# Performance work log

Hardware: AMD Instinct MI355X
Metric: run time of the kernel (lower is better)

Reference implementation:

```python
import math
import jax, jax.numpy as jnp
import numpy as np

H = 1024
NH = 16
HD = H // NH
FF = 4096


def gelu_erf(x):
    return x * 0.5 * (1.0 + jax.lax.erf(x / jnp.sqrt(jnp.float32(2.0))))


def layernorm(x, gamma, beta, eps=1e-12):
    mean = x.mean(axis=-1, keepdims=True)
    var = ((x - mean) ** 2).mean(axis=-1, keepdims=True)
    return gamma * (x - mean) / jnp.sqrt(var + eps) + beta


def setup_inputs() -> dict:
    key = jax.random.key(0)
    ks = jax.random.split(key, 12)
    B, S = 2, 2048
    sc = 0.02
    return {
        "x": jax.random.normal(ks[0], (B, S, H), jnp.float32),
        "attention_mask": jnp.ones((B, S), jnp.int32),
        "Wq": jax.random.normal(ks[1], (H, H), jnp.float32) * sc,
        "bq": jnp.zeros((H,), jnp.float32),
        "Wk": jax.random.normal(ks[2], (H, H), jnp.float32) * sc,
        "bk": jnp.zeros((H,), jnp.float32),
        "Wv": jax.random.normal(ks[3], (H, H), jnp.float32) * sc,
        "bv": jnp.zeros((H,), jnp.float32),
        "Wo": jax.random.normal(ks[4], (H, H), jnp.float32) * sc,
        "bo": jnp.zeros((H,), jnp.float32),
        "ln1_g": jnp.ones((H,), jnp.float32),
        "ln1_b": jnp.zeros((H,), jnp.float32),
        "W1": jax.random.normal(ks[5], (H, FF), jnp.float32) * sc,
        "b1": jnp.zeros((FF,), jnp.float32),
        "W2": jax.random.normal(ks[6], (FF, H), jnp.float32) * sc,
        "b2": jnp.zeros((H,), jnp.float32),
        "ln2_g": jnp.ones((H,), jnp.float32),
        "ln2_b": jnp.zeros((H,), jnp.float32),
    }


def reference(x, attention_mask, Wq, bq, Wk, bk, Wv, bv, Wo, bo,
              ln1_g, ln1_b, W1, b1, W2, b2, ln2_g, ln2_b):
    B, S, _ = x.shape
    # QKV projections, split heads -> [B, NH, S, HD]
    def split(t):
        return t.reshape(B, S, NH, HD).transpose(0, 2, 1, 3)
    q = split(x @ Wq + bq)
    k = split(x @ Wk + bk)
    v = split(x @ Wv + bv)
    # scores [B, NH, S, S]
    s = jnp.einsum("bhqd,bhkd->bhqk", q, k) / math.sqrt(HD)
    mask = (attention_mask == 1)[:, None, None, :]  # [B,1,1,S]
    s = jnp.where(mask, s, -jnp.inf)
    p = jax.nn.softmax(s, axis=-1)
    a = jnp.einsum("bhqk,bhkd->bhqd", p, v)
    a = a.transpose(0, 2, 1, 3).reshape(B, S, H)  # merge heads
    a = a @ Wo + bo
    a = layernorm(a, ln1_g, ln1_b)  # NOTE: no residual in source
    m = gelu_erf(a @ W1 + b1) @ W2 + b2
    return layernorm(m, ln2_g, ln2_b)
```

## Files before the change

kernel.cpp:

```cpp
#include <hip/hip_runtime.h>
#include <hip/hip_bf16.h>
#include <math.h>

typedef __bf16 bf16;
typedef __attribute__((ext_vector_type(8))) __bf16 bf16x8;
typedef __attribute__((ext_vector_type(4))) __bf16 bf16x4;
typedef __attribute__((ext_vector_type(2))) __bf16 bf16x2;
typedef __attribute__((ext_vector_type(4))) float f32x4;
typedef __attribute__((ext_vector_type(4))) short short4v;

#define HDIM 1024
#define NHEAD 16
#define HD 64
#define FFDIM 4096
#define BATCH 2
#define SEQ 2048
#define M_TOK 4096
#define NSPLIT 4
#define PSTRIDE ((size_t)M_TOK * HDIM)

static __device__ __forceinline__ void async_load16(const bf16* g, bf16* l) {
  __builtin_amdgcn_global_load_lds(
      (const __attribute__((address_space(1))) void*)g,
      (__attribute__((address_space(3))) void*)l, 16, 0, 0);
}

static __device__ __forceinline__ f32x4 mfma16_bf16(bf16x4 a, bf16x4 b, f32x4 c) {
#if defined(__HIP_DEVICE_COMPILE__)
#if __has_builtin(__builtin_amdgcn_mfma_f32_16x16x16bf16_1k)
  return __builtin_amdgcn_mfma_f32_16x16x16bf16_1k(
      __builtin_bit_cast(short4v, a), __builtin_bit_cast(short4v, b), c, 0, 0, 0);
#else
  return __builtin_amdgcn_mfma_f32_16x16x16_bf16(a, b, c, 0, 0, 0);
#endif
#else
  return c;
#endif
}

__global__ __launch_bounds__(256)
void prep_kernel(const float* __restrict__ x,
                 const float* __restrict__ Wq, const float* __restrict__ Wk,
                 const float* __restrict__ Wv, const float* __restrict__ Wo,
                 const float* __restrict__ W1, const float* __restrict__ W2,
                 bf16* __restrict__ Xb, bf16* __restrict__ QKVT,
                 bf16* __restrict__ W1T, bf16* __restrict__ W2T)
{
  const int z = blockIdx.z;
  const int t = threadIdx.x;
  if (z == 12) {
    const size_t base = ((size_t)(blockIdx.y * 32 + blockIdx.x)) * 4096;
#pragma unroll
    for (int j = 0; j < 4; ++j) {
      const size_t i = base + j * 1024 + t * 4;
      f32x4 v = *(const f32x4*)(x + i);
      bf16x4 o;
#pragma unroll
      for (int k = 0; k < 4; ++k) o[k] = (bf16)v[k];
      *(bf16x4*)(Xb + i) = o;
    }
    return;
  }
  const float* ps; bf16* pd; int sld, dld;
  if (z < 4) {
    ps = (z == 0) ? Wq : (z == 1) ? Wk : (z == 2) ? Wv : Wo;
    pd = QKVT + (size_t)z * HDIM * HDIM; sld = 1024; dld = 1024;
  } else if (z < 8) {
    const int c = z - 4;
    ps = W1 + c * 1024; sld = 4096;
    pd = W1T + (size_t)c * 1024 * 1024; dld = 1024;
  } else {
    const int c = z - 8;
    ps = W2 + (size_t)c * 1024 * 1024; sld = 1024;
    pd = W2T + c * 1024; dld = 4096;
  }
  __shared__ float tile[32][33];
  const int tx = t & 31, ty = t >> 5;
  const int c0 = blockIdx.x * 32, r0 = blockIdx.y * 32;
#pragma unroll
  for (int i = 0; i < 32; i += 8)
    tile[ty + i][tx] = ps[(size_t)(r0 + ty + i) * sld + c0 + tx];
  __syncthreads();
  const int rr0 = (t & 15) * 2;
  const int ccb = t >> 4;
#pragma unroll
  for (int i = 0; i < 2; ++i) {
    const int cc = ccb + 16 * i;
    bf16x2 v = {(bf16)tile[rr0][cc], (bf16)tile[rr0 + 1][cc]};
    *(bf16x2*)(pd + (size_t)(c0 + cc) * dld + r0 + rr0) = v;
  }
}

template<int EPI>
__global__ __launch_bounds__(256)
void gemm_bt(const bf16* __restrict__ A, const bf16* __restrict__ Bt,
             const float* __restrict__ b0, const float* __restrict__ b1p,
             const float* __restrict__ b2p, void* __restrict__ Cout,
             int M, int N, int ldk, int kchunk)
{
  __shared__ __align__(16) bf16 As[128 * 64];
  __shared__ __align__(16) bf16 Bs[128 * 64];
  const int t = threadIdx.x;
  const int wave = t >> 6, lane = t & 63;
  const int lm = lane & 15, qd = lane >> 4;
  const int wm = (wave >> 1) * 64, wn = (wave & 1) * 64;
  const int bm = blockIdx.y * 128, bn = blockIdx.x * 128;
  const int kbeg = blockIdx.z * kchunk;

  f32x4 acc[4][4] = {};
  const int srow = t >> 3;
  const int schk = t & 7;

  for (int k0 = kbeg; k0 < kbeg + kchunk; k0 += 64) {
#pragma unroll
    for (int r = 0; r < 4; ++r) {
      const int row = r * 32 + srow;
      const int chunk = schk ^ (row & 7);
      async_load16(A + (size_t)(bm + row) * ldk + (k0 + chunk * 8),
                   (bf16*)((char*)As + r * 4096 + t * 16));
    }
#pragma unroll
    for (int r = 0; r < 4; ++r) {
      const int row = r * 32 + srow;
      const int chunk = schk ^ (row & 7);
      async_load16(Bt + (size_t)(bn + row) * ldk + (k0 + chunk * 8),
                   (bf16*)((char*)Bs + r * 4096 + t * 16));
    }
    __syncthreads();
#pragma unroll
    for (int ks = 0; ks < 2; ++ks) {
      bf16x8 av[4], bv[4];
#pragma unroll
      for (int mt = 0; mt < 4; ++mt) {
        const int row = wm + mt * 16 + lm;
        const int chunk = (ks * 4 + qd) ^ (row & 7);
        av[mt] = *(const bf16x8*)(As + row * 64 + chunk * 8);
      }
#pragma unroll
      for (int nt = 0; nt < 4; ++nt) {
        const int row = wn + nt * 16 + lm;
        const int chunk = (ks * 4 + qd) ^ (row & 7);
        bv[nt] = *(const bf16x8*)(Bs + row * 64 + chunk * 8);
      }
#pragma unroll
      for (int mt = 0; mt < 4; ++mt)
#pragma unroll
        for (int nt = 0; nt < 4; ++nt)
          acc[mt][nt] = __builtin_amdgcn_mfma_f32_16x16x32_bf16(bv[nt], av[mt], acc[mt][nt], 0, 0, 0);
    }
    __syncthreads();
  }

#pragma unroll
  for (int nt = 0; nt < 4; ++nt) {
    const int n0 = bn + wn + nt * 16 + qd * 4;
    f32x4 bsv = {0.f, 0.f, 0.f, 0.f};
    if (EPI == 2) bsv = *(const f32x4*)(b0 + n0);
    if (EPI == 3) {
      const int sect = n0 >> 10, c = n0 & 1023;
      const float* bp = (sect == 0) ? b0 : (sect == 1) ? b1p : b2p;
      bsv = *(const f32x4*)(bp + c);
    }
#pragma unroll
    for (int mt = 0; mt < 4; ++mt) {
      const int m = bm + wm + mt * 16 + lm;
      f32x4 v;
#pragma unroll
      for (int r = 0; r < 4; ++r) v[r] = acc[mt][nt][r] + bsv[r];
      if (EPI == 1) {
        bf16x4 o;
#pragma unroll
        for (int r = 0; r < 4; ++r) o[r] = (bf16)v[r];
        *(bf16x4*)((bf16*)Cout + (size_t)blockIdx.z * M * N + (size_t)m * N + n0) = o;
      } else if (EPI == 2) {
        bf16x4 o;
#pragma unroll
        for (int r = 0; r < 4; ++r) {
          const float z = v[r] * 0.70710678118f;
          const float az = fabsf(z);
          const float tt = __builtin_amdgcn_rcpf(fmaf(az, 0.3275911f, 1.0f));
          const float poly = tt * fmaf(tt, fmaf(tt, fmaf(tt, fmaf(tt, 1.061405429f,
                             -1.453152027f), 1.421413741f), -0.284496736f), 0.254829592f);
          const float e = __builtin_amdgcn_exp2f(az * az * -1.4426950408889634f);
          float erfv = 1.0f - poly * e;
          erfv = (z < 0.f) ? -erfv : erfv;
          o[r] = (bf16)(0.5f * v[r] * (1.0f + erfv));
        }
        *(bf16x4*)((bf16*)Cout + (size_t)m * N + n0) = o;
      } else {
        bf16* base = (bf16*)Cout;
        const int sect = n0 >> 10, c = n0 & 1023;
        if (sect < 2) {
          bf16x4 o;
#pragma unroll
          for (int r = 0; r < 4; ++r) o[r] = (bf16)v[r];
          *(bf16x4*)(base + (size_t)sect * M_TOK * HDIM + (size_t)m * HDIM + c) = o;
        } else {
          const int hh = c >> 6, dd = c & 63;
          const int bb = m >> 11, ss = m & 2047;
#pragma unroll
          for (int r = 0; r < 4; ++r)
            base[(size_t)2 * M_TOK * HDIM +
                 (size_t)((bb * NHEAD + hh) * HD + dd + r) * SEQ + ss] = (bf16)v[r];
        }
      }
    }
  }
}

__global__ __launch_bounds__(256)
void attn_kernel(const bf16* __restrict__ Q, const bf16* __restrict__ Kg,
                 const bf16* __restrict__ Vt, const int* __restrict__ mask,
                 bf16* __restrict__ Po, float* __restrict__ Lp)
{
  __shared__ __align__(16) bf16 Ks[64 * 64];
  __shared__ __align__(16) bf16 Vs[64 * 64];
  __shared__ float madd[64];

  const int t = threadIdx.x;
  const int wave = t >> 6, lane = t & 63;
  const int lm = lane & 15, qd = lane >> 4;

  const int lin = blockIdx.x;
  const int g = (lin & 7) * 16 + (lin >> 7);
  const int qblk = (lin >> 3) & 15;
  const int bh = g >> 2;
  const int split = g & 3;
  const int b = bh >> 4, h = bh & 15;
  const int q0 = qblk * 128 + wave * 32;
  const int kv_beg = split * (SEQ / NSPLIT);

  bf16x8 qf[2][2];
#pragma unroll
  for (int qt = 0; qt < 2; ++qt)
#pragma unroll
    for (int ks = 0; ks < 2; ++ks)
      qf[qt][ks] = *(const bf16x8*)(Q + (size_t)(b * SEQ + q0 + qt * 16 + lm) * HDIM +
                                    h * HD + ks * 32 + qd * 8);

  const bf16 onev = (bf16)1.0f;
  const bf16x4 ones = {onev, onev, onev, onev};
  f32x4 lacc[2] = {};
  f32x4 oacc[2][4] = {};

  const int srow = t >> 3, schk = t & 7;
  const float C = 0.1803368801f;

  for (int kv0 = kv_beg; kv0 < kv_beg + SEQ / NSPLIT; kv0 += 64) {
#pragma unroll
    for (int r = 0; r < 2; ++r) {
      const int row = r * 32 + srow;
      const int g2 = schk ^ (row & 7);
      async_load16(Kg + (size_t)(b * SEQ + kv0 + row) * HDIM + h * HD + g2 * 8,
                   (bf16*)((char*)Ks + r * 4096 + t * 16));
      async_load16(Vt + (size_t)(bh * HD + row) * SEQ + kv0 + g2 * 8,
                   (bf16*)((char*)Vs + r * 4096 + t * 16));
    }
    if (t < 64) madd[t] = (mask[b * SEQ + kv0 + t] == 1) ? 0.f : -1.0e30f;
    __syncthreads();

    bf16x8 kf[2][4];
#pragma unroll
    for (int ks = 0; ks < 2; ++ks)
#pragma unroll
      for (int nt = 0; nt < 4; ++nt) {
        const int row = nt * 16 + lm;
        const int c = (ks * 4 + qd) ^ (row & 7);
        kf[ks][nt] = *(const bf16x8*)(Ks + row * 64 + c * 8);
      }

    bf16x4 pf[2][4];
#pragma unroll
    for (int qt = 0; qt < 2; ++qt) {
      f32x4 sacc[4] = {};
#pragma unroll
      for (int ks = 0; ks < 2; ++ks)
#pragma unroll
        for (int nt = 0; nt < 4; ++nt)
          sacc[nt] = __builtin_amdgcn_mfma_f32_16x16x32_bf16(kf[ks][nt], qf[qt][ks], sacc[nt], 0, 0, 0);
#pragma unroll
      for (int nt = 0; nt < 4; ++nt) {
        f32x4 ma = *(const f32x4*)(madd + nt * 16 + qd * 4);
#pragma unroll
        for (int r = 0; r < 4; ++r)
          pf[qt][nt][r] = (bf16)__builtin_amdgcn_exp2f(fmaf(sacc[nt][r], C, ma[r]));
        lacc[qt] = mfma16_bf16(ones, pf[qt][nt], lacc[qt]);
      }
    }

#pragma unroll
    for (int nt2 = 0; nt2 < 4; ++nt2) {
      const int row = nt2 * 16 + lm;
#pragma unroll
      for (int nt = 0; nt < 4; ++nt) {
        bf16x4 vf = *(const bf16x4*)(Vs + row * 64 +
                     (((nt * 2 + (qd >> 1)) ^ (row & 7)) * 8) + (qd & 1) * 4);
        oacc[0][nt2] = mfma16_bf16(vf, pf[0][nt], oacc[0][nt2]);
        oacc[1][nt2] = mfma16_bf16(vf, pf[1][nt], oacc[1][nt2]);
      }
    }
    __syncthreads();
  }

  bf16* po = Po + (size_t)(split * 32 + bh) * 64 * SEQ;
#pragma unroll
  for (int qt = 0; qt < 2; ++qt) {
#pragma unroll
    for (int nt2 = 0; nt2 < 4; ++nt2)
#pragma unroll
      for (int r = 0; r < 4; ++r)
        po[(size_t)(nt2 * 16 + qd * 4 + r) * SEQ + q0 + qt * 16 + lm] =
            (bf16)oacc[qt][nt2][r];
    if (qd == 0)
      Lp[(size_t)(split * 32 + bh) * SEQ + q0 + qt * 16 + lm] = lacc[qt][0];
  }
}

__global__ __launch_bounds__(256)
void attn_merge(const bf16* __restrict__ Po, const float* __restrict__ Lp,
                bf16* __restrict__ Aout)
{
  __shared__ bf16 tile[64][80];
  __shared__ float linv[64];
  const int t = threadIdx.x;
  const int bh = blockIdx.y;
  const int b = bh >> 4, h = bh & 15;
  const int s0 = blockIdx.x * 64;

  if (t < 64) {
    float l = 0.f;
#pragma unroll
    for (int s = 0; s < NSPLIT; ++s)
      l += Lp[(size_t)(s * 32 + bh) * SEQ + s0 + t];
    linv[t] = 1.0f / l;
  }
  __syncthreads();

#pragma unroll
  for (int it = 0; it < 2; ++it) {
    const int d = (t >> 3) + 32 * it;
    const int sc = (t & 7) * 8;
    float acc[8] = {};
#pragma unroll
    for (int s = 0; s < NSPLIT; ++s) {
      bf16x8 v = *(const bf16x8*)(Po + ((size_t)(s * 32 + bh) * 64 + d) * SEQ + s0 + sc);
#pragma unroll
      for (int j = 0; j < 8; ++j) acc[j] += (float)v[j];
    }
#pragma unroll
    for (int j = 0; j < 8; ++j)
      tile[sc + j][d] = (bf16)(acc[j] * linv[sc + j]);
  }
  __syncthreads();

  const int tok = t >> 2, dc = (t & 3) * 16;
  bf16x8 o0 = *(const bf16x8*)&tile[tok][dc];
  bf16x8 o1 = *(const bf16x8*)&tile[tok][dc + 8];
  bf16* dst = Aout + (size_t)(b * SEQ + s0 + tok) * HDIM + h * HD + dc;
  *(bf16x8*)dst = o0;
  *(bf16x8*)(dst + 8) = o1;
}

template<int NP, int OUT_BF16>
__global__ __launch_bounds__(256)
void ln_sum(const bf16* __restrict__ p, const float* __restrict__ bias,
            const float* __restrict__ gamma, const float* __restrict__ beta,
            void* __restrict__ out)
{
  const int row = blockIdx.x;
  const int t = threadIdx.x;
  f32x4 v = {0.f, 0.f, 0.f, 0.f};
#pragma unroll
  for (int np = 0; np < NP; ++np) {
    bf16x4 u = *(const bf16x4*)(p + np * PSTRIDE + (size_t)row * HDIM + t * 4);
#pragma unroll
    for (int j = 0; j < 4; ++j) v[j] += (float)u[j];
  }
  f32x4 bv0 = *(const f32x4*)(bias + t * 4);
#pragma unroll
  for (int j = 0; j < 4; ++j) v[j] += bv0[j];

  float s = v[0] + v[1] + v[2] + v[3];
  float s2 = v[0] * v[0] + v[1] * v[1] + v[2] * v[2] + v[3] * v[3];
#pragma unroll
  for (int d = 1; d < 64; d <<= 1) { s += __shfl_xor(s, d, 64); s2 += __shfl_xor(s2, d, 64); }
  __shared__ float ss[4], ss2[4];
  const int wave = t >> 6, lane = t & 63;
  if (lane == 0) { ss[wave] = s; ss2[wave] = s2; }
  __syncthreads();
  s = ss[0] + ss[1] + ss[2] + ss[3];
  s2 = ss2[0] + ss2[1] + ss2[2] + ss2[3];
  const float mean = s * (1.0f / HDIM);
  const float var = s2 * (1.0f / HDIM) - mean * mean;
  const float rstd = rsqrtf(var + 1e-12f);
  f32x4 gv = *(const f32x4*)(gamma + t * 4);
  f32x4 bv = *(const f32x4*)(beta + t * 4);
  f32x4 y;
#pragma unroll
  for (int j = 0; j < 4; ++j) y[j] = gv[j] * (v[j] - mean) * rstd + bv[j];
  if (OUT_BF16) {
    bf16x4 o;
#pragma unroll
    for (int j = 0; j < 4; ++j) o[j] = (bf16)y[j];
    *(bf16x4*)((bf16*)out + (size_t)row * HDIM + t * 4) = o;
  } else {
    *(f32x4*)((float*)out + (size_t)row * HDIM + t * 4) = y;
  }
}

extern "C" void kernel_launch(void* const* d_in, const int* in_sizes, int n_in,
                              void* d_out, int out_size, void* d_ws, size_t ws_size,
                              hipStream_t stream)
{
  const float* x    = (const float*)d_in[0];
  const int*   am   = (const int*)d_in[1];
  const float* Wq   = (const float*)d_in[2];
  const float* bq   = (const float*)d_in[3];
  const float* Wk   = (const float*)d_in[4];
  const float* bk   = (const float*)d_in[5];
  const float* Wv   = (const float*)d_in[6];
  const float* bv   = (const float*)d_in[7];
  const float* Wo   = (const float*)d_in[8];
  const float* bo   = (const float*)d_in[9];
  const float* ln1g = (const float*)d_in[10];
  const float* ln1b = (const float*)d_in[11];
  const float* W1   = (const float*)d_in[12];
  const float* b1   = (const float*)d_in[13];
  const float* W2   = (const float*)d_in[14];
  const float* b2   = (const float*)d_in[15];
  const float* ln2g = (const float*)d_in[16];
  const float* ln2b = (const float*)d_in[17];

  char* ws = (char*)d_ws;
  const size_t MB = 1ull << 20;
  bf16*  W1T  = (bf16*)(ws + 0 * MB);
  bf16*  W2T  = (bf16*)(ws + 8 * MB);
  bf16*  Xb   = (bf16*)(ws + 16 * MB);
  bf16*  QKVT = (bf16*)(ws + 24 * MB);
  bf16*  WoT  = QKVT + (size_t)3 * HDIM * HDIM;
  bf16*  Qb   = (bf16*)(ws + 33 * MB);
  bf16*  Kb   = (bf16*)(ws + 41 * MB);
  bf16*  Vtb  = (bf16*)(ws + 49 * MB);
  bf16*  Po   = (bf16*)(ws + 57 * MB);
  float* Lp   = (float*)(ws + 89 * MB);
  bf16*  Ab   = (bf16*)(ws + 16 * MB);
  bf16*  Pw   = (bf16*)(ws + 33 * MB);
  bf16*  L1   = (bf16*)(ws + 65 * MB);
  bf16*  F1   = (bf16*)(ws + 16 * MB);
  bf16*  Pf   = (bf16*)(ws + 48 * MB);

  prep_kernel<<<dim3(32, 32, 13), 256, 0, stream>>>(x, Wq, Wk, Wv, Wo, W1, W2,
                                                    Xb, QKVT, W1T, W2T);

  gemm_bt<3><<<dim3(3072 / 128, M_TOK / 128, 1), 256, 0, stream>>>(
      Xb, QKVT, bq, bk, bv, Qb, M_TOK, 3072, HDIM, HDIM);

  attn_kernel<<<dim3(2048, 1, 1), 256, 0, stream>>>(Qb, Kb, Vtb, am, Po, Lp);
  attn_merge<<<dim3(SEQ / 64, BATCH * NHEAD), 256, 0, stream>>>(Po, Lp, Ab);

  gemm_bt<1><<<dim3(HDIM / 128, M_TOK / 128, 2), 256, 0, stream>>>(
      Ab, WoT, nullptr, nullptr, nullptr, Pw, M_TOK, HDIM, HDIM, 512);
  ln_sum<2, 1><<<M_TOK, 256, 0, stream>>>(Pw, bo, ln1g, ln1b, L1);

  gemm_bt<2><<<dim3(FFDIM / 128, M_TOK / 128, 1), 256, 0, stream>>>(
      L1, W1T, b1, nullptr, nullptr, F1, M_TOK, FFDIM, HDIM, HDIM);

  gemm_bt<1><<<dim3(HDIM / 128, M_TOK / 128, 4), 256, 0, stream>>>(
      F1, W2T, nullptr, nullptr, nullptr, Pf, M_TOK, HDIM, FFDIM, 1024);
  ln_sum<4, 0><<<M_TOK, 256, 0, stream>>>(Pf, b2, ln2g, ln2b, (float*)d_out);
}
```

Baseline: 362.2 us.

## Replace 128x128 GEMM with double-buffered 256x256 pipelined MFMA kernel

Replaces the single-buffered 128x128 GEMM with a 512-thread kernel that computes 256x256 output tiles. It double-buffers LDS and interleaves async global-to-LDS staging of the next K-tile with four MFMA phases, using explicit barriers, vmcnt waits and s_setprio. The larger tiles raise operand reuse and the overlap hides load latency behind math. In exchange, grids shrink to 128–256 blocks, which may underfill the 256 CUs (especially the Wo projection). The 128KB of LDS per block also limits residency to one block per CU.

```diff
diff --git a/kernel.cpp b/kernel.cpp
--- a/kernel.cpp
+++ b/kernel.cpp
@@ -91,69 +91,126 @@
   }
 }
 
+
+#define STAGE_Q(OP, BASEMN, LDSB, KOFF, Q) do { \
+    const int rr_ = (Q) * 64 + (t >> 3); \
+    const int gc_ = (t & 7) ^ (rr_ & 7); \
+    async_load16((OP) + (size_t)((BASEMN) + rr_) * ldk + (KOFF) + gc_ * 8, \
+                 (LDSB) + (Q) * 4096 + t * 8); \
+  } while (0)
+
+#define STAGE_HALF(OP, BASEMN, LDSB, KOFF, H) do { \
+    STAGE_Q(OP, BASEMN, LDSB, KOFF, 2 * (H)); \
+    STAGE_Q(OP, BASEMN, LDSB, KOFF, 2 * (H) + 1); \
+  } while (0)
+
+#define LOAD_AV(BUF, MH) do { \
+    _Pragma("unroll") \
+    for (int mt_ = 0; mt_ < 4; ++mt_) { \
+      const int row_ = wm + (MH) * 64 + mt_ * 16 + lm; \
+      _Pragma("unroll") \
+      for (int ks_ = 0; ks_ < 2; ++ks_) { \
+        const int c_ = (ks_ * 4 + qd) ^ (row_ & 7); \
+        av[mt_][ks_] = *(const bf16x8*)(As_[BUF] + row_ * 64 + c_ * 8); \
+      } \
+    } \
+  } while (0)
+
+#define LOAD_BV(DST, BUF, NH) do { \
+    _Pragma("unroll") \
+    for (int nt_ = 0; nt_ < 2; ++nt_) { \
+      const int row_ = wnb + (NH) * 32 + nt_ * 16 + lm; \
+      _Pragma("unroll") \
+      for (int ks_ = 0; ks_ < 2; ++ks_) { \
+        const int c_ = (ks_ * 4 + qd) ^ (row_ & 7); \
+        DST[nt_][ks_] = *(const bf16x8*)(Bs_[BUF] + row_ * 64 + c_ * 8); \
+      } \
+    } \
+  } while (0)
+
+#define MFMA_Q(MH, BV, NH) do { \
+    __builtin_amdgcn_s_setprio(1); \
+    _Pragma("unroll") \
+    for (int mt_ = 0; mt_ < 4; ++mt_) \
+      _Pragma("unroll") \
+      for (int nt_ = 0; nt_ < 2; ++nt_) \
+        _Pragma("unroll") \
+        for (int ks_ = 0; ks_ < 2; ++ks_) \
+          acc[(MH) * 4 + mt_][(NH) * 2 + nt_] = \
+              __builtin_amdgcn_mfma_f32_16x16x32_bf16( \
+                  BV[nt_][ks_], av[mt_][ks_], \
+                  acc[(MH) * 4 + mt_][(NH) * 2 + nt_], 0, 0, 0); \
+    __builtin_amdgcn_s_setprio(0); \
+  } while (0)
+
+#define BARX() do { \
+    __builtin_amdgcn_sched_barrier(0); \
+    __builtin_amdgcn_s_barrier(); \
+    __builtin_amdgcn_sched_barrier(0); \
+  } while (0)
+
+#define VMCNT4() asm volatile("s_waitcnt vmcnt(4)" ::: "memory")
+
+#define FOURPH(RB, WAB, KTA, WBB, KTB) do { \
+     \
+    LOAD_AV(RB, 0); LOAD_BV(bv0, RB, 0); \
+    STAGE_HALF(A, bm, As_[WAB], kbeg + (KTA) * 64, 0); \
+    BARX(); MFMA_Q(0, bv0, 0); BARX(); \
+     \
+    LOAD_BV(bv1, RB, 1); \
+    STAGE_HALF(A, bm, As_[WAB], kbeg + (KTA) * 64, 1); \
+    BARX(); MFMA_Q(0, bv1, 1); BARX(); \
+     \
+    LOAD_AV(RB, 1); \
+    STAGE_HALF(Bt, bn, Bs_[WBB], kbeg + (KTB) * 64, 0); \
+    BARX(); MFMA_Q(1, bv0, 0); BARX(); \
+     \
+    STAGE_HALF(Bt, bn, Bs_[WBB], kbeg + (KTB) * 64, 1); \
+    BARX(); MFMA_Q(1, bv1, 1); VMCNT4(); BARX(); \
+  } while (0)
+
 template<int EPI>
-__global__ __launch_bounds__(256)
-void gemm_bt(const bf16* __restrict__ A, const bf16* __restrict__ Bt,
+__global__ __launch_bounds__(512, 2)
+void gemm256(const bf16* __restrict__ A, const bf16* __restrict__ Bt,
              const float* __restrict__ b0, const float* __restrict__ b1p,
              const float* __restrict__ b2p, void* __restrict__ Cout,
              int M, int N, int ldk, int kchunk)
 {
-  __shared__ __align__(16) bf16 As[128 * 64];
-  __shared__ __align__(16) bf16 Bs[128 * 64];
+  __shared__ __align__(16) bf16 As_[2][256 * 64];
+  __shared__ __align__(16) bf16 Bs_[2][256 * 64];
+
   const int t = threadIdx.x;
   const int wave = t >> 6, lane = t & 63;
   const int lm = lane & 15, qd = lane >> 4;
-  const int wm = (wave >> 1) * 64, wn = (wave & 1) * 64;
-  const int bm = blockIdx.y * 128, bn = blockIdx.x * 128;
+  const int wm = (wave >> 2) * 128;
+  const int wnb = (wave & 3) * 64;
+  const int bm = blockIdx.y * 256, bn = blockIdx.x * 256;
   const int kbeg = blockIdx.z * kchunk;
-
-  f32x4 acc[4][4] = {};
-  const int srow = t >> 3;
-  const int schk = t & 7;
-
-  for (int k0 = kbeg; k0 < kbeg + kchunk; k0 += 64) {
-#pragma unroll
-    for (int r = 0; r < 4; ++r) {
-      const int row = r * 32 + srow;
-      const int chunk = schk ^ (row & 7);
-      async_load16(A + (size_t)(bm + row) * ldk + (k0 + chunk * 8),
-                   (bf16*)((char*)As + r * 4096 + t * 16));
-    }
-#pragma unroll
-    for (int r = 0; r < 4; ++r) {
-      const int row = r * 32 + srow;
-      const int chunk = schk ^ (row & 7);
-      async_load16(Bt + (size_t)(bn + row) * ldk + (k0 + chunk * 8),
-                   (bf16*)((char*)Bs + r * 4096 + t * 16));
-    }
-    __syncthreads();
-#pragma unroll
-    for (int ks = 0; ks < 2; ++ks) {
-      bf16x8 av[4], bv[4];
-#pragma unroll
-      for (int mt = 0; mt < 4; ++mt) {
-        const int row = wm + mt * 16 + lm;
-        const int chunk = (ks * 4 + qd) ^ (row & 7);
-        av[mt] = *(const bf16x8*)(As + row * 64 + chunk * 8);
-      }
-#pragma unroll
-      for (int nt = 0; nt < 4; ++nt) {
-        const int row = wn + nt * 16 + lm;
-        const int chunk = (ks * 4 + qd) ^ (row & 7);
-        bv[nt] = *(const bf16x8*)(Bs + row * 64 + chunk * 8);
-      }
-#pragma unroll
-      for (int mt = 0; mt < 4; ++mt)
-#pragma unroll
-        for (int nt = 0; nt < 4; ++nt)
-          acc[mt][nt] = __builtin_amdgcn_mfma_f32_16x16x32_bf16(bv[nt], av[mt], acc[mt][nt], 0, 0, 0);
-    }
-    __syncthreads();
-  }
-
-#pragma unroll
-  for (int nt = 0; nt < 4; ++nt) {
-    const int n0 = bn + wn + nt * 16 + qd * 4;
+  const int NT = kchunk >> 6;
+
+  f32x4 acc[8][4] = {};
+  bf16x8 av[4][2], bv0[2][2], bv1[2][2];
+
+  STAGE_HALF(Bt, bn, Bs_[0], kbeg, 0);
+  STAGE_HALF(Bt, bn, Bs_[0], kbeg, 1);
+  STAGE_HALF(A,  bm, As_[0], kbeg, 0);
+  STAGE_HALF(A,  bm, As_[0], kbeg, 1);
+  STAGE_HALF(Bt, bn, Bs_[1], kbeg + 64, 0);
+  STAGE_HALF(Bt, bn, Bs_[1], kbeg + 64, 1);
+  VMCNT4();
+  BARX();
+
+  for (int it = 0; it < NT / 2; ++it) {
+    const int tb = 2 * it + 1;
+    const int tc = (2 * it + 2) & (NT - 1);
+    const int td = (2 * it + 3) & (NT - 1);
+    FOURPH(0, 1, tb, 0, tc);
+    FOURPH(1, 0, tc, 1, td);
+  }
+
+#pragma unroll
+  for (int nt4 = 0; nt4 < 4; ++nt4) {
+    const int n0 = bn + wnb + nt4 * 16 + qd * 4;
     f32x4 bsv = {0.f, 0.f, 0.f, 0.f};
     if (EPI == 2) bsv = *(const f32x4*)(b0 + n0);
     if (EPI == 3) {
@@ -162,11 +219,11 @@
       bsv = *(const f32x4*)(bp + c);
     }
 #pragma unroll
-    for (int mt = 0; mt < 4; ++mt) {
-      const int m = bm + wm + mt * 16 + lm;
+    for (int mt8 = 0; mt8 < 8; ++mt8) {
+      const int m = bm + wm + mt8 * 16 + lm;
       f32x4 v;
 #pragma unroll
-      for (int r = 0; r < 4; ++r) v[r] = acc[mt][nt][r] + bsv[r];
+      for (int r = 0; r < 4; ++r) v[r] = acc[mt8][nt4][r] + bsv[r];
       if (EPI == 1) {
         bf16x4 o;
 #pragma unroll
@@ -452,20 +509,20 @@
   prep_kernel<<<dim3(32, 32, 13), 256, 0, stream>>>(x, Wq, Wk, Wv, Wo, W1, W2,
                                                     Xb, QKVT, W1T, W2T);
 
-  gemm_bt<3><<<dim3(3072 / 128, M_TOK / 128, 1), 256, 0, stream>>>(
+  gemm256<3><<<dim3(3072 / 256, M_TOK / 256, 1), 512, 0, stream>>>(
       Xb, QKVT, bq, bk, bv, Qb, M_TOK, 3072, HDIM, HDIM);
 
   attn_kernel<<<dim3(2048, 1, 1), 256, 0, stream>>>(Qb, Kb, Vtb, am, Po, Lp);
   attn_merge<<<dim3(SEQ / 64, BATCH * NHEAD), 256, 0, stream>>>(Po, Lp, Ab);
 
-  gemm_bt<1><<<dim3(HDIM / 128, M_TOK / 128, 2), 256, 0, stream>>>(
+  gemm256<1><<<dim3(HDIM / 256, M_TOK / 256, 2), 512, 0, stream>>>(
       Ab, WoT, nullptr, nullptr, nullptr, Pw, M_TOK, HDIM, HDIM, 512);
   ln_sum<2, 1><<<M_TOK, 256, 0, stream>>>(Pw, bo, ln1g, ln1b, L1);
 
-  gemm_bt<2><<<dim3(FFDIM / 128, M_TOK / 128, 1), 256, 0, stream>>>(
+  gemm256<2><<<dim3(FFDIM / 256, M_TOK / 256, 1), 512, 0, stream>>>(
       L1, W1T, b1, nullptr, nullptr, F1, M_TOK, FFDIM, HDIM, HDIM);
 
-  gemm_bt<1><<<dim3(HDIM / 128, M_TOK / 128, 4), 256, 0, stream>>>(
+  gemm256<1><<<dim3(HDIM / 256, M_TOK / 256, 4), 512, 0, stream>>>(
       F1, W2T, nullptr, nullptr, nullptr, Pf, M_TOK, HDIM, FFDIM, 1024);
   ln_sum<4, 0><<<M_TOK, 256, 0, stream>>>(Pf, b2, ln2g, ln2b, (float*)d_out);
 }
```

Measured after the change: 358.2 us. About the same (-1.1%).

## Stage GEMM epilogue through LDS, halve attention KV splits, add MFMA priority hints

Applied to the files above, without the earlier changes.

The GEMM epilogue now writes each wave's 64x64 output tile into shared memory first, then stores it to global memory as full 16-byte rows. This includes the transposed V layout, which previously used scattered 2-byte stores. Attention drops from four KV splits to two, halving the grid and the partial outputs that the merge step must read. s_setprio is raised around the MFMA sections to favour matrix issue. The risks are lower attention parallelism from the smaller grid, and extra LDS traffic plus possible bank conflicts in the epilogue.

```diff
diff --git a/kernel.cpp b/kernel.cpp
--- a/kernel.cpp
+++ b/kernel.cpp
@@ -16,7 +16,7 @@
 #define BATCH 2
 #define SEQ 2048
 #define M_TOK 4096
-#define NSPLIT 4
+#define NSPLIT 2
 #define PSTRIDE ((size_t)M_TOK * HDIM)
 
 static __device__ __forceinline__ void async_load16(const bf16* g, bf16* l) {
@@ -98,8 +98,9 @@
              const float* __restrict__ b2p, void* __restrict__ Cout,
              int M, int N, int ldk, int kchunk)
 {
-  __shared__ __align__(16) bf16 As[128 * 64];
-  __shared__ __align__(16) bf16 Bs[128 * 64];
+  __shared__ __align__(16) bf16 Smem[2][128 * 64];
+  bf16* As = Smem[0];
+  bf16* Bs = Smem[1];
   const int t = threadIdx.x;
   const int wave = t >> 6, lane = t & 63;
   const int lm = lane & 15, qd = lane >> 4;
@@ -150,6 +151,9 @@
     }
     __syncthreads();
   }
+
+  bf16* tw = &Smem[0][0] + wave * 4096;
+  const bool vt = (EPI == 3) && ((bn + wn) >= 2 * HDIM);
 
 #pragma unroll
   for (int nt = 0; nt < 4; ++nt) {
@@ -163,17 +167,11 @@
     }
 #pragma unroll
     for (int mt = 0; mt < 4; ++mt) {
-      const int m = bm + wm + mt * 16 + lm;
       f32x4 v;
 #pragma unroll
       for (int r = 0; r < 4; ++r) v[r] = acc[mt][nt][r] + bsv[r];
-      if (EPI == 1) {
-        bf16x4 o;
-#pragma unroll
-        for (int r = 0; r < 4; ++r) o[r] = (bf16)v[r];
-        *(bf16x4*)((bf16*)Cout + (size_t)blockIdx.z * M * N + (size_t)m * N + n0) = o;
-      } else if (EPI == 2) {
-        bf16x4 o;
+      bf16x4 o;
+      if (EPI == 2) {
 #pragma unroll
         for (int r = 0; r < 4; ++r) {
           const float z = v[r] * 0.70710678118f;
@@ -186,23 +184,60 @@
           erfv = (z < 0.f) ? -erfv : erfv;
           o[r] = (bf16)(0.5f * v[r] * (1.0f + erfv));
         }
-        *(bf16x4*)((bf16*)Cout + (size_t)m * N + n0) = o;
       } else {
-        bf16* base = (bf16*)Cout;
-        const int sect = n0 >> 10, c = n0 & 1023;
-        if (sect < 2) {
-          bf16x4 o;
-#pragma unroll
-          for (int r = 0; r < 4; ++r) o[r] = (bf16)v[r];
-          *(bf16x4*)(base + (size_t)sect * M_TOK * HDIM + (size_t)m * HDIM + c) = o;
-        } else {
-          const int hh = c >> 6, dd = c & 63;
-          const int bb = m >> 11, ss = m & 2047;
-#pragma unroll
-          for (int r = 0; r < 4; ++r)
-            base[(size_t)2 * M_TOK * HDIM +
-                 (size_t)((bb * NHEAD + hh) * HD + dd + r) * SEQ + ss] = (bf16)v[r];
-        }
+#pragma unroll
+        for (int r = 0; r < 4; ++r) o[r] = (bf16)v[r];
+      }
+      if (!vt) {
+        *(bf16x4*)(tw + (mt * 16 + lm) * 64 + nt * 16 + qd * 4) = o;
+      } else {
+#pragma unroll
+        for (int r = 0; r < 4; ++r)
+          tw[(nt * 16 + qd * 4 + r) * 64 + mt * 16 + lm] = o[r];
+      }
+    }
+  }
+  const int erow = lane >> 3, ech = lane & 7;
+  if (EPI == 1) {
+    bf16* dst = (bf16*)Cout + (size_t)blockIdx.z * M * N +
+                (size_t)(bm + wm) * N + (bn + wn);
+#pragma unroll
+    for (int p = 0; p < 8; ++p) {
+      const int row = p * 8 + erow;
+      bf16x8 val = *(const bf16x8*)(tw + row * 64 + ech * 8);
+      *(bf16x8*)(dst + (size_t)row * N + ech * 8) = val;
+    }
+  } else if (EPI == 2) {
+    bf16* dst = (bf16*)Cout + (size_t)(bm + wm) * N + (bn + wn);
+#pragma unroll
+    for (int p = 0; p < 8; ++p) {
+      const int row = p * 8 + erow;
+      bf16x8 val = *(const bf16x8*)(tw + row * 64 + ech * 8);
+      *(bf16x8*)(dst + (size_t)row * N + ech * 8) = val;
+    }
+  } else {
+    bf16* base = (bf16*)Cout;
+    const int sect = (bn + wn) >> 10;
+    if (!vt) {
+      bf16* dst = base + (size_t)sect * M_TOK * HDIM +
+                  (size_t)(bm + wm) * HDIM + ((bn + wn) & 1023);
+#pragma unroll
+      for (int p = 0; p < 8; ++p) {
+        const int row = p * 8 + erow;
+        bf16x8 val = *(const bf16x8*)(tw + row * 64 + ech * 8);
+        *(bf16x8*)(dst + (size_t)row * HDIM + ech * 8) = val;
+      }
+    } else {
+      const int c0 = (bn + wn) & 1023;
+      const int hh = c0 >> 6;
+      const int bb = (bm + wm) >> 11, ss0 = (bm + wm) & 2047;
+      bf16* dst = base + (size_t)2 * M_TOK * HDIM +
+                  (size_t)((bb * NHEAD + hh) * HD) * SEQ + ss0;
+#pragma unroll
+      for (int p = 0; p < 8; ++p) {
+        const int row = p * 8 + erow;
+        bf16x8 val = *(const bf16x8*)(tw + row * 64 + ech * 8);
+        *(bf16x8*)(dst + (size_t)row * SEQ + ech * 8) = val;
       }
     }
   }
@@ -222,10 +257,10 @@
   const int lm = lane & 15, qd = lane >> 4;
 
   const int lin = blockIdx.x;
-  const int g = (lin & 7) * 16 + (lin >> 7);
+  const int g = (lin & 7) * 8 + (lin >> 7);
   const int qblk = (lin >> 3) & 15;
-  const int bh = g >> 2;
-  const int split = g & 3;
+  const int bh = g >> 1;
+  const int split = g & 1;
   const int b = bh >> 4, h = bh & 15;
   const int q0 = qblk * 128 + wave * 32;
   const int kv_beg = split * (SEQ / NSPLIT);
@@ -273,11 +308,13 @@
 #pragma unroll
     for (int qt = 0; qt < 2; ++qt) {
       f32x4 sacc[4] = {};
+      __builtin_amdgcn_s_setprio(1);
 #pragma unroll
       for (int ks = 0; ks < 2; ++ks)
 #pragma unroll
         for (int nt = 0; nt < 4; ++nt)
           sacc[nt] = __builtin_amdgcn_mfma_f32_16x16x32_bf16(kf[ks][nt], qf[qt][ks], sacc[nt], 0, 0, 0);
+      __builtin_amdgcn_s_setprio(0);
 #pragma unroll
       for (int nt = 0; nt < 4; ++nt) {
         f32x4 ma = *(const f32x4*)(madd + nt * 16 + qd * 4);
@@ -288,6 +325,7 @@
       }
     }
 
+    __builtin_amdgcn_s_setprio(1);
 #pragma unroll
     for (int nt2 = 0; nt2 < 4; ++nt2) {
       const int row = nt2 * 16 + lm;
@@ -299,6 +337,7 @@
         oacc[1][nt2] = mfma16_bf16(vf, pf[1][nt], oacc[1][nt2]);
       }
     }
+    __builtin_amdgcn_s_setprio(0);
     __syncthreads();
   }
 
@@ -455,7 +494,7 @@
   gemm_bt<3><<<dim3(3072 / 128, M_TOK / 128, 1), 256, 0, stream>>>(
       Xb, QKVT, bq, bk, bv, Qb, M_TOK, 3072, HDIM, HDIM);
 
-  attn_kernel<<<dim3(2048, 1, 1), 256, 0, stream>>>(Qb, Kb, Vtb, am, Po, Lp);
+  attn_kernel<<<dim3(1024, 1, 1), 256, 0, stream>>>(Qb, Kb, Vtb, am, Po, Lp);
   attn_merge<<<dim3(SEQ / 64, BATCH * NHEAD), 256, 0, stream>>>(Po, Lp, Ab);
 
   gemm_bt<1><<<dim3(HDIM / 128, M_TOK / 128, 2), 256, 0, stream>>>(
```

Result: no change. 363.4 us (+0.4%).
